# Kernel tuning notes

Hardware: AMD Instinct MI355X
Metric: run time of the kernel (lower is better)

Reference implementation:

```python
import jax, jax.numpy as jnp
import numpy as np


def gcn_conv(h, edge_index, num_nodes):
    # Symmetric-normalized GCN aggregation: out[i] = sum_{(j->i)} h[j] / sqrt(deg(i)*deg(j))
    row, col = edge_index[0], edge_index[1]
    deg = jax.ops.segment_sum(jnp.ones(col.shape, dtype=h.dtype), col, num_segments=num_nodes)
    d_inv_sqrt = jnp.where(deg > 0, jax.lax.rsqrt(jnp.maximum(deg, 1.0)), 0.0)
    w = d_inv_sqrt[row] * d_inv_sqrt[col]           # [E]
    msg = h[row] * w[:, None]                        # [E, D] gather + scale
    return jax.ops.segment_sum(msg, col, num_segments=num_nodes)  # [N, D] scatter-add


def setup_inputs() -> dict:
    key = jax.random.key(0)
    k1, k2, k3, k4 = jax.random.split(key, 4)
    N, E, F_IN, F_HID, F_OUT = 100000, 1600000, 128, 64, 40
    x = jax.random.normal(k1, (N, F_IN), dtype=jnp.float32)
    edge_index = jax.random.randint(k2, (2, E), 0, N, dtype=jnp.int64)
    # xavier_uniform with gain=1.414 (as in reset_parameters); biases zero
    def xavier(k, shape, gain=1.414):
        fan_out, fan_in = shape
        a = gain * np.sqrt(6.0 / (fan_in + fan_out))
        return jax.random.uniform(k, shape, jnp.float32, -a, a)
    W1 = xavier(k3, (F_HID, F_IN))
    b1 = jnp.zeros((F_HID,), dtype=jnp.float32)
    W2 = xavier(k4, (F_OUT, F_HID))
    b2 = jnp.zeros((F_OUT,), dtype=jnp.float32)
    return {"x": x, "edge_index": edge_index, "W1": W1, "b1": b1, "W2": W2, "b2": b2}


def reference(x, edge_index, W1, b1, W2, b2):
    # GNN.forward with num_layers=2, use_mp=True, eval mode (dropout inactive)
    N = x.shape[0]
    h = x @ W1.T                      # [N, nhid]
    h = gcn_conv(h, edge_index, N)
    h = jax.nn.relu(h + b1)
    h = h @ W2.T                      # [N, nclass]
    h = gcn_conv(h, edge_index, N)
    return h + b2
```

## Files before the change

kernel.cpp:

```cpp
#include <hip/hip_runtime.h>
#include <hip/hip_fp16.h>


typedef __attribute__((ext_vector_type(8))) _Float16 half8v;
typedef __attribute__((ext_vector_type(4))) float   float4v;

__global__ void k_binfill(const int* __restrict__ ed,
                          int* __restrict__ gbincnt, unsigned* __restrict__ binbuf,
                          int E, int cap) {
  __shared__ int hist[512];
  __shared__ int cursor[512];
  __shared__ unsigned rec[4096];
  __shared__ unsigned short binv[4096];
  __shared__ int s_is64;
  int t = threadIdx.x;
  hist[t] = 0; hist[t + 256] = 0;
  if (t == 0) s_is64 = 1;
  __syncthreads();
  {
    int any = 0;
    #pragma unroll
    for (int u = 0; u < 8; ++u) {
      int idx = 2 * (t * 8 + u) + 1;
      if (idx < 2 * E && ed[idx] != 0) any = 1;
    }
    if (any) s_is64 = 0;
  }
  __syncthreads();
  const int is64 = s_is64;
  const int base = blockIdx.x * 4096;
  const int nE = min(4096, E - base);
  for (int j = t; j < nE; j += 256) {
    int e = base + j;
    int r = is64 ? ed[2 * e] : ed[e];
    int c = is64 ? ed[2 * (E + e)] : ed[E + e];
    rec[j] = (unsigned)r | ((unsigned)(c & 255) << 17);
    binv[j] = (unsigned short)(c >> 8);
    atomicAdd(&hist[c >> 8], 1);
  }
  __syncthreads();
  for (int b = t; b < 512; b += 256) {
    int h = hist[b];
    cursor[b] = h ? atomicAdd(&gbincnt[b], h) : 0;
  }
  __syncthreads();
  for (int j = t; j < nE; j += 256) {
    int bin = binv[j];
    int pos = atomicAdd(&cursor[bin], 1);
    if (pos < cap)
      binbuf[(size_t)bin * cap + pos] = rec[j];
  }
}

__global__ void k_degscat(const unsigned* __restrict__ binbuf, const int* __restrict__ gbincnt,
                          float* __restrict__ dis, int* __restrict__ rowptr,
                          int* __restrict__ srcs, int NBINS, int N, int cap) {
  __shared__ int sd[512];
  __shared__ int cnt[256];
  __shared__ int sc[256];
  __shared__ int cursor[256];
  __shared__ unsigned rec[8192];
  int t = threadIdx.x, b = blockIdx.x;
  sd[t]       = (t < NBINS)       ? min(gbincnt[t], cap)       : 0;
  sd[t + 256] = (t + 256 < NBINS) ? min(gbincnt[t + 256], cap) : 0;
  cnt[t] = 0;
  __syncthreads();
  for (int off = 1; off < 512; off <<= 1) {
    int v0 = (t >= off) ? sd[t - off] : 0;
    int v1 = sd[t + 256 - off];
    __syncthreads();
    sd[t] += v0; sd[t + 256] += v1;
    __syncthreads();
  }
  const int mybase = (b == 0) ? 0 : sd[b - 1];
  if (b == NBINS - 1 && t == 0) rowptr[N] = sd[NBINS - 1];

  int n = min(gbincnt[b], cap);
  const unsigned* buf = binbuf + (size_t)b * cap;
  for (int j = t; j < n; j += 256) {
    unsigned v = buf[j];
    rec[j] = v;
    atomicAdd(&cnt[v >> 17], 1);
  }
  __syncthreads();
  sc[t] = cnt[t];
  __syncthreads();
  for (int off = 1; off < 256; off <<= 1) {
    int v = (t >= off) ? sc[t - off] : 0;
    __syncthreads();
    sc[t] += v;
    __syncthreads();
  }
  int rp = mybase + ((t == 0) ? 0 : sc[t - 1]);
  cursor[t] = rp;
  int node = b * 256 + t;
  if (node < N) {
    int d = cnt[t];
    dis[node] = (d > 0) ? rsqrtf((float)d) : 0.f;
    rowptr[node] = rp;
  }
  __syncthreads();
  for (int j = t; j < n; j += 256) {
    unsigned v = rec[j];
    int pos = atomicAdd(&cursor[v >> 17], 1);
    srcs[pos] = (int)(v & 0x1FFFF);
  }
}

__launch_bounds__(256)
__global__ void k_gemm1_mfma(const float* __restrict__ X, const float* __restrict__ W,
                             const float* __restrict__ dis, unsigned char* __restrict__ h1q,
                             float* __restrict__ sc1, int N) {
  __shared__ _Float16 xl[128 * 128];
  __shared__ _Float16 wl[64 * 128];
  const int t = threadIdx.x;
  const int row0 = blockIdx.x * 128;

  #pragma unroll
  for (int j = 0; j < 8; ++j) {
    int qq = t + 256 * j;
    int r = qq >> 5, k4 = qq & 31;
    float4 v = *(const float4*)&W[(size_t)r * 128 + k4 * 4];
    _Float16 h4[4] = {(_Float16)v.x, (_Float16)v.y, (_Float16)v.z, (_Float16)v.w};
    int k = (k4 * 4) ^ ((r & 7) * 8);
    *(float2*)&wl[r * 128 + k] = *(float2*)h4;
  }
  #pragma unroll
  for (int j = 0; j < 16; ++j) {
    int qq = t + 256 * j;
    int r = qq >> 5, k4 = qq & 31;
    int row = row0 + r;
    float4 v = make_float4(0.f, 0.f, 0.f, 0.f);
    if (row < N) v = *(const float4*)&X[(size_t)row * 128 + k4 * 4];
    _Float16 h4[4] = {(_Float16)v.x, (_Float16)v.y, (_Float16)v.z, (_Float16)v.w};
    int k = (k4 * 4) ^ ((r & 7) * 8);
    *(float2*)&xl[r * 128 + k] = *(float2*)h4;
  }
  __syncthreads();

  const int w = t >> 6, l = t & 63;
  const int m0 = w * 32;
  const int lr = l & 15, q = l >> 4;

  float4v acc[2][4] = {};
  #pragma unroll
  for (int kc = 0; kc < 4; ++kc) {
    half8v a[2], b[4];
    #pragma unroll
    for (int mt = 0; mt < 2; ++mt) {
      int m = m0 + mt * 16 + lr;
      int k = (kc * 32 + q * 8) ^ ((m & 7) * 8);
      a[mt] = *(half8v*)&xl[m * 128 + k];
    }
    #pragma unroll
    for (int nt = 0; nt < 4; ++nt) {
      int n = nt * 16 + lr;
      int k = (kc * 32 + q * 8) ^ ((n & 7) * 8);
      b[nt] = *(half8v*)&wl[n * 128 + k];
    }
    #pragma unroll
    for (int mt = 0; mt < 2; ++mt)
      #pragma unroll
      for (int nt = 0; nt < 4; ++nt)
        acc[mt][nt] = __builtin_amdgcn_mfma_f32_16x16x32_f16(a[mt], b[nt], acc[mt][nt], 0, 0, 0);
  }

  #pragma unroll
  for (int mt = 0; mt < 2; ++mt) {
    #pragma unroll
    for (int r = 0; r < 4; ++r) {
      int row = row0 + m0 + mt * 16 + q * 4 + r;
      if (row < N) {
        float dr = dis[row];
        float v0 = acc[mt][0][r] * dr;
        float v1 = acc[mt][1][r] * dr;
        float v2 = acc[mt][2][r] * dr;
        float v3 = acc[mt][3][r] * dr;
        float m = fmaxf(fmaxf(fabsf(v0), fabsf(v1)), fmaxf(fabsf(v2), fabsf(v3)));
        #pragma unroll
        for (int off = 1; off < 16; off <<= 1)
          m = fmaxf(m, __shfl_xor(m, off));
        float inv = (m > 0.f) ? (127.f / m) : 0.f;
        unsigned char* dst = h1q + (size_t)row * 64;
        int q0 = (int)rintf(v0 * inv);
        int q1 = (int)rintf(v1 * inv);
        int q2 = (int)rintf(v2 * inv);
        int q3 = (int)rintf(v3 * inv);
        q0 = max(-127, min(127, q0));
        q1 = max(-127, min(127, q1));
        q2 = max(-127, min(127, q2));
        q3 = max(-127, min(127, q3));
        dst[lr]      = (unsigned char)(signed char)q0;
        dst[lr + 16] = (unsigned char)(signed char)q1;
        dst[lr + 32] = (unsigned char)(signed char)q2;
        dst[lr + 48] = (unsigned char)(signed char)q3;
        if (lr == 0) sc1[row] = m * (1.f / 127.f);
      }
    }
  }
}

__launch_bounds__(256)
__global__ void k_gemm2_mfma(const __half* __restrict__ Xh, const float* __restrict__ W,
                             const float* __restrict__ dis, unsigned char* __restrict__ h2,
                             int N) {
  __shared__ _Float16 xl[128 * 64];
  __shared__ _Float16 wl[48 * 64];
  const int t = threadIdx.x;
  const int row0 = blockIdx.x * 128;

  for (int i = t; i < 48 * 8; i += 256) {
    int c = i >> 3, kq = i & 7;
    _Float16 h8[8];
    #pragma unroll
    for (int j = 0; j < 8; ++j)
      h8[j] = (c < 40) ? (_Float16)W[c * 64 + kq * 8 + j] : (_Float16)0.f;
    *(float4*)&wl[c * 64 + ((kq * 8) ^ ((c & 7) * 8))] = *(float4*)h8;
  }
  for (int i = t; i < 1024; i += 256) {
    int r = i >> 3, kq = i & 7;
    int row = row0 + r;
    float4 v = make_float4(0.f, 0.f, 0.f, 0.f);
    if (row < N) v = *(const float4*)&Xh[(size_t)row * 64 + kq * 8];
    *(float4*)&xl[r * 64 + ((kq * 8) ^ ((r & 7) * 8))] = v;
  }
  __syncthreads();

  const int w = t >> 6, l = t & 63;
  const int m0 = w * 32;
  const int lr = l & 15, q = l >> 4;

  float4v acc[2][3] = {};
  #pragma unroll
  for (int kc = 0; kc < 2; ++kc) {
    half8v a[2], b[3];
    #pragma unroll
    for (int mt = 0; mt < 2; ++mt) {
      int m = m0 + mt * 16 + lr;
      int k = (kc * 32 + q * 8) ^ ((m & 7) * 8);
      a[mt] = *(half8v*)&xl[m * 64 + k];
    }
    #pragma unroll
    for (int nt = 0; nt < 3; ++nt) {
      int n = nt * 16 + lr;
      int k = (kc * 32 + q * 8) ^ ((n & 7) * 8);
      b[nt] = *(half8v*)&wl[n * 64 + k];
    }
    #pragma unroll
    for (int mt = 0; mt < 2; ++mt)
      #pragma unroll
      for (int nt = 0; nt < 3; ++nt)
        acc[mt][nt] = __builtin_amdgcn_mfma_f32_16x16x32_f16(a[mt], b[nt], acc[mt][nt], 0, 0, 0);
  }

  #pragma unroll
  for (int mt = 0; mt < 2; ++mt) {
    #pragma unroll
    for (int r = 0; r < 4; ++r) {
      int row = row0 + m0 + mt * 16 + q * 4 + r;
      if (row < N) {
        float dr = dis[row];
        float v0 = acc[mt][0][r] * dr;
        float v1 = acc[mt][1][r] * dr;
        float v2 = acc[mt][2][r] * dr;
        float m = fmaxf(fabsf(v0), fmaxf(fabsf(v1), fabsf(v2)));
        #pragma unroll
        for (int off = 1; off < 16; off <<= 1)
          m = fmaxf(m, __shfl_xor(m, off));
        float s = m * (1.f / 127.f);
        float inv = (m > 0.f) ? (127.f / m) : 0.f;
        unsigned char* dst = h2 + (size_t)row * 64;
        int q0 = (int)rintf(v0 * inv);
        int q1 = (int)rintf(v1 * inv);
        int q2 = (int)rintf(v2 * inv);
        q0 = max(-127, min(127, q0));
        q1 = max(-127, min(127, q1));
        q2 = max(-127, min(127, q2));
        dst[lr]      = (unsigned char)(signed char)q0;
        dst[lr + 16] = (unsigned char)(signed char)q1;
        if (lr + 32 < 40) dst[lr + 32] = (unsigned char)(signed char)q2;
        if (lr == 0) *(float*)&dst[40] = s;
        if (lr >= 1 && lr <= 5) *(int*)&dst[40 + 4 * lr] = 0;
      }
    }
  }
}

__launch_bounds__(256)
__global__ void k_conv64(const unsigned char* __restrict__ H, const float* __restrict__ sc1,
                         const int* __restrict__ rowptr, const int* __restrict__ srcs,
                         const float* __restrict__ dis, const float* __restrict__ b1,
                         __half* __restrict__ out, int N) {
  int node = blockIdx.x * 4 + (threadIdx.x >> 6);
  if (node >= N) return;
  int lane = threadIdx.x & 63;
  int g = lane >> 3, li = lane & 7;
  int s = rowptr[node], e = rowptr[node + 1];
  int last = e - 1;
  float a0 = 0.f, a1 = 0.f, a2 = 0.f, a3 = 0.f,
        a4 = 0.f, a5 = 0.f, a6 = 0.f, a7 = 0.f;
  for (int p = s; p < e; p += 32) {
    int sv = srcs[min(p + (lane & 31), last)];
    #pragma unroll
    for (int u = 0; u < 4; ++u) {
      if (p + 8 * u >= e) break;
      int src = __shfl(sv, 8 * u + g);
      uint2 raw = *(const uint2*)&H[(size_t)src * 64 + 8 * li];
      float sc = sc1[src];
      if (p + 8 * u + g < e) {
        int x0 = (int)raw.x, x1 = (int)raw.y;
        a0 = fmaf((float)((x0 << 24) >> 24), sc, a0);
        a1 = fmaf((float)((x0 << 16) >> 24), sc, a1);
        a2 = fmaf((float)((x0 << 8)  >> 24), sc, a2);
        a3 = fmaf((float)( x0        >> 24), sc, a3);
        a4 = fmaf((float)((x1 << 24) >> 24), sc, a4);
        a5 = fmaf((float)((x1 << 16) >> 24), sc, a5);
        a6 = fmaf((float)((x1 << 8)  >> 24), sc, a6);
        a7 = fmaf((float)( x1        >> 24), sc, a7);
      }
    }
  }
  #pragma unroll
  for (int off = 8; off <= 32; off <<= 1) {
    a0 += __shfl_xor(a0, off); a1 += __shfl_xor(a1, off);
    a2 += __shfl_xor(a2, off); a3 += __shfl_xor(a3, off);
    a4 += __shfl_xor(a4, off); a5 += __shfl_xor(a5, off);
    a6 += __shfl_xor(a6, off); a7 += __shfl_xor(a7, off);
  }
  if (g == 0) {
    float dn = dis[node];
    const float* bb = b1 + 8 * li;
    __half hv[8];
    hv[0] = __float2half_rn(fmaxf(fmaf(a0, dn, bb[0]), 0.f));
    hv[1] = __float2half_rn(fmaxf(fmaf(a1, dn, bb[1]), 0.f));
    hv[2] = __float2half_rn(fmaxf(fmaf(a2, dn, bb[2]), 0.f));
    hv[3] = __float2half_rn(fmaxf(fmaf(a3, dn, bb[3]), 0.f));
    hv[4] = __float2half_rn(fmaxf(fmaf(a4, dn, bb[4]), 0.f));
    hv[5] = __float2half_rn(fmaxf(fmaf(a5, dn, bb[5]), 0.f));
    hv[6] = __float2half_rn(fmaxf(fmaf(a6, dn, bb[6]), 0.f));
    hv[7] = __float2half_rn(fmaxf(fmaf(a7, dn, bb[7]), 0.f));
    *(float4*)&out[(size_t)node * 64 + 8 * li] = *(float4*)hv;
  }
}

__launch_bounds__(256)
__global__ void k_conv40(const unsigned char* __restrict__ H, const int* __restrict__ rowptr,
                         const int* __restrict__ srcs, const float* __restrict__ dis,
                         const float* __restrict__ b2, float* __restrict__ out, int N) {
  int node = blockIdx.x * 4 + (threadIdx.x >> 6);
  if (node >= N) return;
  int lane = threadIdx.x & 63;
  int g = lane >> 3, li = lane & 7;
  bool act = li < 5;
  int s = rowptr[node], e = rowptr[node + 1];
  int last = e - 1;
  float a0 = 0.f, a1 = 0.f, a2 = 0.f, a3 = 0.f,
        a4 = 0.f, a5 = 0.f, a6 = 0.f, a7 = 0.f;
  for (int p = s; p < e; p += 32) {
    int sv = srcs[min(p + (lane & 31), last)];
    #pragma unroll
    for (int u = 0; u < 4; ++u) {
      if (p + 8 * u >= e) break;
      int src = __shfl(sv, 8 * u + g);
      if (act) {
        const unsigned char* rowp = &H[(size_t)src * 64];
        uint2 raw = *(const uint2*)&rowp[8 * li];
        float sc = *(const float*)&rowp[40];
        if (p + 8 * u + g < e) {
          int x0 = (int)raw.x, x1 = (int)raw.y;
          a0 = fmaf((float)((x0 << 24) >> 24), sc, a0);
          a1 = fmaf((float)((x0 << 16) >> 24), sc, a1);
          a2 = fmaf((float)((x0 << 8)  >> 24), sc, a2);
          a3 = fmaf((float)( x0        >> 24), sc, a3);
          a4 = fmaf((float)((x1 << 24) >> 24), sc, a4);
          a5 = fmaf((float)((x1 << 16) >> 24), sc, a5);
          a6 = fmaf((float)((x1 << 8)  >> 24), sc, a6);
          a7 = fmaf((float)( x1        >> 24), sc, a7);
        }
      }
    }
  }
  #pragma unroll
  for (int off = 8; off <= 32; off <<= 1) {
    a0 += __shfl_xor(a0, off); a1 += __shfl_xor(a1, off);
    a2 += __shfl_xor(a2, off); a3 += __shfl_xor(a3, off);
    a4 += __shfl_xor(a4, off); a5 += __shfl_xor(a5, off);
    a6 += __shfl_xor(a6, off); a7 += __shfl_xor(a7, off);
  }
  if (g == 0 && act) {
    float dn = dis[node];
    const float* bb = b2 + 8 * li;
    float4 v0 = make_float4(fmaf(a0, dn, bb[0]), fmaf(a1, dn, bb[1]),
                            fmaf(a2, dn, bb[2]), fmaf(a3, dn, bb[3]));
    float4 v1 = make_float4(fmaf(a4, dn, bb[4]), fmaf(a5, dn, bb[5]),
                            fmaf(a6, dn, bb[6]), fmaf(a7, dn, bb[7]));
    *(float4*)&out[(size_t)node * 40 + 8 * li] = v0;
    *(float4*)&out[(size_t)node * 40 + 8 * li + 4] = v1;
  }
}

extern "C" void kernel_launch(void* const* d_in, const int* in_sizes, int n_in,
                              void* d_out, int out_size, void* d_ws, size_t ws_size,
                              hipStream_t stream) {
  const float* x  = (const float*)d_in[0];
  const int*   ed = (const int*)d_in[1];
  const float* W1 = (const float*)d_in[2];
  const float* b1 = (const float*)d_in[3];
  const float* W2 = (const float*)d_in[4];
  const float* b2 = (const float*)d_in[5];
  float* out = (float*)d_out;

  const int FIN = 128, FH = 64;
  const int N = in_sizes[0] / FIN;
  const int E = in_sizes[1] / 2;
  const int NBINS = (N + 255) >> 8;

  char* ws = (char*)d_ws;
  size_t off = 0;
  auto alloc = [&](size_t bytes) {
    void* p = ws + off;
    off = (off + bytes + 255) & ~(size_t)255;
    return p;
  };
  int*           gbincnt = (int*)alloc(512 * 4);
  float*         dis     = (float*)alloc((size_t)N * 4);
  int*           rowptr  = (int*)alloc(((size_t)N + 1) * 4);
  int*           srcs    = (int*)alloc((size_t)E * 4);
  unsigned char* h1q     = (unsigned char*)alloc((size_t)N * FH * 2);
  __half*        h1b     = (__half*)alloc((size_t)N * FH * 2);
  unsigned char* h2      = (unsigned char*)alloc((size_t)N * 64);
  float* sc1 = (float*)(h1q + (((size_t)N * 64 + 255) & ~(size_t)255));
  int cap = (int)(((size_t)N * FH * 2) / ((size_t)NBINS * 4));
  if (cap > 8192) cap = 8192;
  unsigned* binbuf = (unsigned*)h1q;

  hipMemsetAsync(gbincnt, 0, 512 * 4, stream);

  int fb = (E + 4095) / 4096;
  k_binfill<<<fb, 256, 0, stream>>>(ed, gbincnt, binbuf, E, cap);
  k_degscat<<<NBINS, 256, 0, stream>>>(binbuf, gbincnt, dis, rowptr, srcs, NBINS, N, cap);

  int mb = (N + 127) / 128;
  int cb = (N + 3) / 4;
  k_gemm1_mfma<<<mb, 256, 0, stream>>>(x, W1, dis, h1q, sc1, N);
  k_conv64<<<cb, 256, 0, stream>>>(h1q, sc1, rowptr, srcs, dis, b1, h1b, N);
  k_gemm2_mfma<<<mb, 256, 0, stream>>>(h1b, W2, dis, h2, N);
  k_conv40<<<cb, 256, 0, stream>>>(h2, rowptr, srcs, dis, b2, out, N);
}
```

Baseline: 253.7 us.

## Assign one 8-lane group per node in GCN aggregation kernels

Both aggregation kernels now map each node to 8 lanes instead of a full 64-lane wavefront. Each group walks its edge list 4 at a time with direct index loads, and the cross-group shuffle reduction is gone. With about 16 edges per node, the old scheme left most of the 8 groups idle in the tail of each 32-edge chunk and spent time on shuffles. The cost is divergence between the 8 nodes sharing a wave when their degrees differ, and less memory parallelism per node.

Measured after the change: 232.6 us. 1.09x faster.

```diff
diff --git a/kernel.cpp b/kernel.cpp
--- a/kernel.cpp
+++ b/kernel.cpp
@@ -291,103 +291,161 @@
                          const int* __restrict__ rowptr, const int* __restrict__ srcs,
                          const float* __restrict__ dis, const float* __restrict__ b1,
                          __half* __restrict__ out, int N) {
-  int node = blockIdx.x * 4 + (threadIdx.x >> 6);
+  int t = threadIdx.x;
+  int li = t & 7;
+  int node = blockIdx.x * 32 + (t >> 3);
   if (node >= N) return;
-  int lane = threadIdx.x & 63;
-  int g = lane >> 3, li = lane & 7;
   int s = rowptr[node], e = rowptr[node + 1];
   int last = e - 1;
   float a0 = 0.f, a1 = 0.f, a2 = 0.f, a3 = 0.f,
         a4 = 0.f, a5 = 0.f, a6 = 0.f, a7 = 0.f;
-  for (int p = s; p < e; p += 32) {
-    int sv = srcs[min(p + (lane & 31), last)];
-    #pragma unroll
-    for (int u = 0; u < 4; ++u) {
-      if (p + 8 * u >= e) break;
-      int src = __shfl(sv, 8 * u + g);
-      uint2 raw = *(const uint2*)&H[(size_t)src * 64 + 8 * li];
-      float sc = sc1[src];
-      if (p + 8 * u + g < e) {
-        int x0 = (int)raw.x, x1 = (int)raw.y;
-        a0 = fmaf((float)((x0 << 24) >> 24), sc, a0);
-        a1 = fmaf((float)((x0 << 16) >> 24), sc, a1);
-        a2 = fmaf((float)((x0 << 8)  >> 24), sc, a2);
-        a3 = fmaf((float)( x0        >> 24), sc, a3);
-        a4 = fmaf((float)((x1 << 24) >> 24), sc, a4);
-        a5 = fmaf((float)((x1 << 16) >> 24), sc, a5);
-        a6 = fmaf((float)((x1 << 8)  >> 24), sc, a6);
-        a7 = fmaf((float)( x1        >> 24), sc, a7);
-      }
-    }
-  }
-  #pragma unroll
-  for (int off = 8; off <= 32; off <<= 1) {
-    a0 += __shfl_xor(a0, off); a1 += __shfl_xor(a1, off);
-    a2 += __shfl_xor(a2, off); a3 += __shfl_xor(a3, off);
-    a4 += __shfl_xor(a4, off); a5 += __shfl_xor(a5, off);
-    a6 += __shfl_xor(a6, off); a7 += __shfl_xor(a7, off);
-  }
-  if (g == 0) {
-    float dn = dis[node];
-    const float* bb = b1 + 8 * li;
-    __half hv[8];
-    hv[0] = __float2half_rn(fmaxf(fmaf(a0, dn, bb[0]), 0.f));
-    hv[1] = __float2half_rn(fmaxf(fmaf(a1, dn, bb[1]), 0.f));
-    hv[2] = __float2half_rn(fmaxf(fmaf(a2, dn, bb[2]), 0.f));
-    hv[3] = __float2half_rn(fmaxf(fmaf(a3, dn, bb[3]), 0.f));
-    hv[4] = __float2half_rn(fmaxf(fmaf(a4, dn, bb[4]), 0.f));
-    hv[5] = __float2half_rn(fmaxf(fmaf(a5, dn, bb[5]), 0.f));
-    hv[6] = __float2half_rn(fmaxf(fmaf(a6, dn, bb[6]), 0.f));
-    hv[7] = __float2half_rn(fmaxf(fmaf(a7, dn, bb[7]), 0.f));
-    *(float4*)&out[(size_t)node * 64 + 8 * li] = *(float4*)hv;
-  }
+  for (int p = s; p < e; p += 4) {
+    int s0 = srcs[p];
+    int s1 = srcs[min(p + 1, last)];
+    int s2 = srcs[min(p + 2, last)];
+    int s3 = srcs[min(p + 3, last)];
+    uint2 r0 = *(const uint2*)&H[(size_t)s0 * 64 + 8 * li];
+    uint2 r1 = *(const uint2*)&H[(size_t)s1 * 64 + 8 * li];
+    uint2 r2 = *(const uint2*)&H[(size_t)s2 * 64 + 8 * li];
+    uint2 r3 = *(const uint2*)&H[(size_t)s3 * 64 + 8 * li];
+    float c0 = sc1[s0], c1 = sc1[s1], c2 = sc1[s2], c3 = sc1[s3];
+    {
+      int x0 = (int)r0.x, x1 = (int)r0.y;
+      a0 = fmaf((float)((x0 << 24) >> 24), c0, a0);
+      a1 = fmaf((float)((x0 << 16) >> 24), c0, a1);
+      a2 = fmaf((float)((x0 << 8)  >> 24), c0, a2);
+      a3 = fmaf((float)( x0        >> 24), c0, a3);
+      a4 = fmaf((float)((x1 << 24) >> 24), c0, a4);
+      a5 = fmaf((float)((x1 << 16) >> 24), c0, a5);
+      a6 = fmaf((float)((x1 << 8)  >> 24), c0, a6);
+      a7 = fmaf((float)( x1        >> 24), c0, a7);
+    }
+    if (p + 1 < e) {
+      int x0 = (int)r1.x, x1 = (int)r1.y;
+      a0 = fmaf((float)((x0 << 24) >> 24), c1, a0);
+      a1 = fmaf((float)((x0 << 16) >> 24), c1, a1);
+      a2 = fmaf((float)((x0 << 8)  >> 24), c1, a2);
+      a3 = fmaf((float)( x0        >> 24), c1, a3);
+      a4 = fmaf((float)((x1 << 24) >> 24), c1, a4);
+      a5 = fmaf((float)((x1 << 16) >> 24), c1, a5);
+      a6 = fmaf((float)((x1 << 8)  >> 24), c1, a6);
+      a7 = fmaf((float)( x1        >> 24), c1, a7);
+    }
+    if (p + 2 < e) {
+      int x0 = (int)r2.x, x1 = (int)r2.y;
+      a0 = fmaf((float)((x0 << 24) >> 24), c2, a0);
+      a1 = fmaf((float)((x0 << 16) >> 24), c2, a1);
+      a2 = fmaf((float)((x0 << 8)  >> 24), c2, a2);
+      a3 = fmaf((float)( x0        >> 24), c2, a3);
+      a4 = fmaf((float)((x1 << 24) >> 24), c2, a4);
+      a5 = fmaf((float)((x1 << 16) >> 24), c2, a5);
+      a6 = fmaf((float)((x1 << 8)  >> 24), c2, a6);
+      a7 = fmaf((float)( x1        >> 24), c2, a7);
+    }
+    if (p + 3 < e) {
+      int x0 = (int)r3.x, x1 = (int)r3.y;
+      a0 = fmaf((float)((x0 << 24) >> 24), c3, a0);
+      a1 = fmaf((float)((x0 << 16) >> 24), c3, a1);
+      a2 = fmaf((float)((x0 << 8)  >> 24), c3, a2);
+      a3 = fmaf((float)( x0        >> 24), c3, a3);
+      a4 = fmaf((float)((x1 << 24) >> 24), c3, a4);
+      a5 = fmaf((float)((x1 << 16) >> 24), c3, a5);
+      a6 = fmaf((float)((x1 << 8)  >> 24), c3, a6);
+      a7 = fmaf((float)( x1        >> 24), c3, a7);
+    }
+  }
+  float dn = dis[node];
+  const float* bb = b1 + 8 * li;
+  __half hv[8];
+  hv[0] = __float2half_rn(fmaxf(fmaf(a0, dn, bb[0]), 0.f));
+  hv[1] = __float2half_rn(fmaxf(fmaf(a1, dn, bb[1]), 0.f));
+  hv[2] = __float2half_rn(fmaxf(fmaf(a2, dn, bb[2]), 0.f));
+  hv[3] = __float2half_rn(fmaxf(fmaf(a3, dn, bb[3]), 0.f));
+  hv[4] = __float2half_rn(fmaxf(fmaf(a4, dn, bb[4]), 0.f));
+  hv[5] = __float2half_rn(fmaxf(fmaf(a5, dn, bb[5]), 0.f));
+  hv[6] = __float2half_rn(fmaxf(fmaf(a6, dn, bb[6]), 0.f));
+  hv[7] = __float2half_rn(fmaxf(fmaf(a7, dn, bb[7]), 0.f));
+  *(float4*)&out[(size_t)node * 64 + 8 * li] = *(float4*)hv;
 }
 
 __launch_bounds__(256)
 __global__ void k_conv40(const unsigned char* __restrict__ H, const int* __restrict__ rowptr,
                          const int* __restrict__ srcs, const float* __restrict__ dis,
                          const float* __restrict__ b2, float* __restrict__ out, int N) {
-  int node = blockIdx.x * 4 + (threadIdx.x >> 6);
+  int t = threadIdx.x;
+  int li = t & 7;
+  int node = blockIdx.x * 32 + (t >> 3);
   if (node >= N) return;
-  int lane = threadIdx.x & 63;
-  int g = lane >> 3, li = lane & 7;
   bool act = li < 5;
   int s = rowptr[node], e = rowptr[node + 1];
   int last = e - 1;
   float a0 = 0.f, a1 = 0.f, a2 = 0.f, a3 = 0.f,
         a4 = 0.f, a5 = 0.f, a6 = 0.f, a7 = 0.f;
-  for (int p = s; p < e; p += 32) {
-    int sv = srcs[min(p + (lane & 31), last)];
-    #pragma unroll
-    for (int u = 0; u < 4; ++u) {
-      if (p + 8 * u >= e) break;
-      int src = __shfl(sv, 8 * u + g);
-      if (act) {
-        const unsigned char* rowp = &H[(size_t)src * 64];
-        uint2 raw = *(const uint2*)&rowp[8 * li];
-        float sc = *(const float*)&rowp[40];
-        if (p + 8 * u + g < e) {
-          int x0 = (int)raw.x, x1 = (int)raw.y;
-          a0 = fmaf((float)((x0 << 24) >> 24), sc, a0);
-          a1 = fmaf((float)((x0 << 16) >> 24), sc, a1);
-          a2 = fmaf((float)((x0 << 8)  >> 24), sc, a2);
-          a3 = fmaf((float)( x0        >> 24), sc, a3);
-          a4 = fmaf((float)((x1 << 24) >> 24), sc, a4);
-          a5 = fmaf((float)((x1 << 16) >> 24), sc, a5);
-          a6 = fmaf((float)((x1 << 8)  >> 24), sc, a6);
-          a7 = fmaf((float)( x1        >> 24), sc, a7);
-        }
+  for (int p = s; p < e; p += 4) {
+    int s0 = srcs[p];
+    int s1 = srcs[min(p + 1, last)];
+    int s2 = srcs[min(p + 2, last)];
+    int s3 = srcs[min(p + 3, last)];
+    if (act) {
+      const unsigned char* p0 = &H[(size_t)s0 * 64];
+      const unsigned char* p1 = &H[(size_t)s1 * 64];
+      const unsigned char* p2 = &H[(size_t)s2 * 64];
+      const unsigned char* p3 = &H[(size_t)s3 * 64];
+      uint2 r0 = *(const uint2*)&p0[8 * li];
+      uint2 r1 = *(const uint2*)&p1[8 * li];
+      uint2 r2 = *(const uint2*)&p2[8 * li];
+      uint2 r3 = *(const uint2*)&p3[8 * li];
+      float c0 = *(const float*)&p0[40];
+      float c1 = *(const float*)&p1[40];
+      float c2 = *(const float*)&p2[40];
+      float c3 = *(const float*)&p3[40];
+      {
+        int x0 = (int)r0.x, x1 = (int)r0.y;
+        a0 = fmaf((float)((x0 << 24) >> 24), c0, a0);
+        a1 = fmaf((float)((x0 << 16) >> 24), c0, a1);
+        a2 = fmaf((float)((x0 << 8)  >> 24), c0, a2);
+        a3 = fmaf((float)( x0        >> 24), c0, a3);
+        a4 = fmaf((float)((x1 << 24) >> 24), c0, a4);
+        a5 = fmaf((float)((x1 << 16) >> 24), c0, a5);
+        a6 = fmaf((float)((x1 << 8)  >> 24), c0, a6);
+        a7 = fmaf((float)( x1        >> 24), c0, a7);
       }
-    }
-  }
-  #pragma unroll
-  for (int off = 8; off <= 32; off <<= 1) {
-    a0 += __shfl_xor(a0, off); a1 += __shfl_xor(a1, off);
-    a2 += __shfl_xor(a2, off); a3 += __shfl_xor(a3, off);
-    a4 += __shfl_xor(a4, off); a5 += __shfl_xor(a5, off);
-    a6 += __shfl_xor(a6, off); a7 += __shfl_xor(a7, off);
-  }
-  if (g == 0 && act) {
+      if (p + 1 < e) {
+        int x0 = (int)r1.x, x1 = (int)r1.y;
+        a0 = fmaf((float)((x0 << 24) >> 24), c1, a0);
+        a1 = fmaf((float)((x0 << 16) >> 24), c1, a1);
+        a2 = fmaf((float)((x0 << 8)  >> 24), c1, a2);
+        a3 = fmaf((float)( x0        >> 24), c1, a3);
+        a4 = fmaf((float)((x1 << 24) >> 24), c1, a4);
+        a5 = fmaf((float)((x1 << 16) >> 24), c1, a5);
+        a6 = fmaf((float)((x1 << 8)  >> 24), c1, a6);
+        a7 = fmaf((float)( x1        >> 24), c1, a7);
+      }
+      if (p + 2 < e) {
+        int x0 = (int)r2.x, x1 = (int)r2.y;
+        a0 = fmaf((float)((x0 << 24) >> 24), c2, a0);
+        a1 = fmaf((float)((x0 << 16) >> 24), c2, a1);
+        a2 = fmaf((float)((x0 << 8)  >> 24), c2, a2);
+        a3 = fmaf((float)( x0        >> 24), c2, a3);
+        a4 = fmaf((float)((x1 << 24) >> 24), c2, a4);
+        a5 = fmaf((float)((x1 << 16) >> 24), c2, a5);
+        a6 = fmaf((float)((x1 << 8)  >> 24), c2, a6);
+        a7 = fmaf((float)( x1        >> 24), c2, a7);
+      }
+      if (p + 3 < e) {
+        int x0 = (int)r3.x, x1 = (int)r3.y;
+        a0 = fmaf((float)((x0 << 24) >> 24), c3, a0);
+        a1 = fmaf((float)((x0 << 16) >> 24), c3, a1);
+        a2 = fmaf((float)((x0 << 8)  >> 24), c3, a2);
+        a3 = fmaf((float)( x0        >> 24), c3, a3);
+        a4 = fmaf((float)((x1 << 24) >> 24), c3, a4);
+        a5 = fmaf((float)((x1 << 16) >> 24), c3, a5);
+        a6 = fmaf((float)((x1 << 8)  >> 24), c3, a6);
+        a7 = fmaf((float)( x1        >> 24), c3, a7);
+      }
+    }
+  }
+  if (act) {
     float dn = dis[node];
     const float* bb = b2 + 8 * li;
     float4 v0 = make_float4(fmaf(a0, dn, bb[0]), fmaf(a1, dn, bb[1]),
@@ -441,7 +499,7 @@
   k_degscat<<<NBINS, 256, 0, stream>>>(binbuf, gbincnt, dis, rowptr, srcs, NBINS, N, cap);
 
   int mb = (N + 127) / 128;
-  int cb = (N + 3) / 4;
+  int cb = (N + 31) / 32;
   k_gemm1_mfma<<<mb, 256, 0, stream>>>(x, W1, dis, h1q, sc1, N);
   k_conv64<<<cb, 256, 0, stream>>>(h1q, sc1, rowptr, srcs, dis, b1, h1b, N);
   k_gemm2_mfma<<<mb, 256, 0, stream>>>(h1b, W2, dis, h2, N);
```

## Assign one 8-lane group per node in conv kernels; load GEMM1 A operands directly

Applied to the files above, without the earlier changes.

The two aggregation kernels now map 8 lanes to each destination node, with 32 nodes per block, where before a full 64-lane wavefront served one node. Each lane walks all of the node's edges in batches of 8 with independent loads, and the cross-group shuffle reduction is removed. This aims to stop wasting lanes on low-degree nodes (average degree about 16) and to raise memory-level parallelism. Separately, GEMM1 loads X rows straight from global memory into registers in MFMA operand layout, skipping the shared-memory staging of X. The costs are higher register pressure and divergence across nodes of different degree within a wavefront.

Result: faster. 219.4 us (-13.5%).

```diff
diff --git a/kernel.cpp b/kernel.cpp
--- a/kernel.cpp
+++ b/kernel.cpp
@@ -111,10 +111,24 @@
 __global__ void k_gemm1_mfma(const float* __restrict__ X, const float* __restrict__ W,
                              const float* __restrict__ dis, unsigned char* __restrict__ h1q,
                              float* __restrict__ sc1, int N) {
-  __shared__ _Float16 xl[128 * 128];
   __shared__ _Float16 wl[64 * 128];
   const int t = threadIdx.x;
   const int row0 = blockIdx.x * 128;
+  const int w = t >> 6, l = t & 63;
+  const int m0 = w * 32;
+  const int lr = l & 15, q = l >> 4;
+
+  float4 xr[4][2][2];
+  #pragma unroll
+  for (int kc = 0; kc < 4; ++kc) {
+    #pragma unroll
+    for (int mt = 0; mt < 2; ++mt) {
+      int row = min(row0 + m0 + mt * 16 + lr, N - 1);
+      const float* p = &X[(size_t)row * 128 + kc * 32 + q * 8];
+      xr[kc][mt][0] = *(const float4*)p;
+      xr[kc][mt][1] = *(const float4*)(p + 4);
+    }
+  }
 
   #pragma unroll
   for (int j = 0; j < 8; ++j) {
@@ -125,22 +139,7 @@
     int k = (k4 * 4) ^ ((r & 7) * 8);
     *(float2*)&wl[r * 128 + k] = *(float2*)h4;
   }
-  #pragma unroll
-  for (int j = 0; j < 16; ++j) {
-    int qq = t + 256 * j;
-    int r = qq >> 5, k4 = qq & 31;
-    int row = row0 + r;
-    float4 v = make_float4(0.f, 0.f, 0.f, 0.f);
-    if (row < N) v = *(const float4*)&X[(size_t)row * 128 + k4 * 4];
-    _Float16 h4[4] = {(_Float16)v.x, (_Float16)v.y, (_Float16)v.z, (_Float16)v.w};
-    int k = (k4 * 4) ^ ((r & 7) * 8);
-    *(float2*)&xl[r * 128 + k] = *(float2*)h4;
-  }
-  __syncthreads();
-
-  const int w = t >> 6, l = t & 63;
-  const int m0 = w * 32;
-  const int lr = l & 15, q = l >> 4;
+  __syncthreads();
 
   float4v acc[2][4] = {};
   #pragma unroll
@@ -148,9 +147,10 @@
     half8v a[2], b[4];
     #pragma unroll
     for (int mt = 0; mt < 2; ++mt) {
-      int m = m0 + mt * 16 + lr;
-      int k = (kc * 32 + q * 8) ^ ((m & 7) * 8);
-      a[mt] = *(half8v*)&xl[m * 128 + k];
+      float4 v0 = xr[kc][mt][0], v1 = xr[kc][mt][1];
+      _Float16 h8[8] = {(_Float16)v0.x, (_Float16)v0.y, (_Float16)v0.z, (_Float16)v0.w,
+                        (_Float16)v1.x, (_Float16)v1.y, (_Float16)v1.z, (_Float16)v1.w};
+      a[mt] = *(half8v*)h8;
     }
     #pragma unroll
     for (int nt = 0; nt < 4; ++nt) {
@@ -291,103 +291,95 @@
                          const int* __restrict__ rowptr, const int* __restrict__ srcs,
                          const float* __restrict__ dis, const float* __restrict__ b1,
                          __half* __restrict__ out, int N) {
-  int node = blockIdx.x * 4 + (threadIdx.x >> 6);
+  int t = threadIdx.x;
+  int li = t & 7;
+  int node = blockIdx.x * 32 + (t >> 3);
   if (node >= N) return;
-  int lane = threadIdx.x & 63;
-  int g = lane >> 3, li = lane & 7;
   int s = rowptr[node], e = rowptr[node + 1];
   int last = e - 1;
   float a0 = 0.f, a1 = 0.f, a2 = 0.f, a3 = 0.f,
         a4 = 0.f, a5 = 0.f, a6 = 0.f, a7 = 0.f;
-  for (int p = s; p < e; p += 32) {
-    int sv = srcs[min(p + (lane & 31), last)];
-    #pragma unroll
-    for (int u = 0; u < 4; ++u) {
-      if (p + 8 * u >= e) break;
-      int src = __shfl(sv, 8 * u + g);
-      uint2 raw = *(const uint2*)&H[(size_t)src * 64 + 8 * li];
-      float sc = sc1[src];
-      if (p + 8 * u + g < e) {
-        int x0 = (int)raw.x, x1 = (int)raw.y;
-        a0 = fmaf((float)((x0 << 24) >> 24), sc, a0);
-        a1 = fmaf((float)((x0 << 16) >> 24), sc, a1);
-        a2 = fmaf((float)((x0 << 8)  >> 24), sc, a2);
-        a3 = fmaf((float)( x0        >> 24), sc, a3);
-        a4 = fmaf((float)((x1 << 24) >> 24), sc, a4);
-        a5 = fmaf((float)((x1 << 16) >> 24), sc, a5);
-        a6 = fmaf((float)((x1 << 8)  >> 24), sc, a6);
-        a7 = fmaf((float)( x1        >> 24), sc, a7);
+  for (int p = s; p < e; p += 8) {
+    int sv[8]; uint2 rv[8]; float cv[8];
+    #pragma unroll
+    for (int u = 0; u < 8; ++u) sv[u] = srcs[min(p + u, last)];
+    #pragma unroll
+    for (int u = 0; u < 8; ++u) rv[u] = *(const uint2*)&H[(size_t)sv[u] * 64 + 8 * li];
+    #pragma unroll
+    for (int u = 0; u < 8; ++u) cv[u] = sc1[sv[u]];
+    #pragma unroll
+    for (int u = 0; u < 8; ++u) {
+      if (p + u < e) {
+        int x0 = (int)rv[u].x, x1 = (int)rv[u].y;
+        float c = cv[u];
+        a0 = fmaf((float)((x0 << 24) >> 24), c, a0);
+        a1 = fmaf((float)((x0 << 16) >> 24), c, a1);
+        a2 = fmaf((float)((x0 << 8)  >> 24), c, a2);
+        a3 = fmaf((float)( x0        >> 24), c, a3);
+        a4 = fmaf((float)((x1 << 24) >> 24), c, a4);
+        a5 = fmaf((float)((x1 << 16) >> 24), c, a5);
+        a6 = fmaf((float)((x1 << 8)  >> 24), c, a6);
+        a7 = fmaf((float)( x1        >> 24), c, a7);
       }
     }
   }
-  #pragma unroll
-  for (int off = 8; off <= 32; off <<= 1) {
-    a0 += __shfl_xor(a0, off); a1 += __shfl_xor(a1, off);
-    a2 += __shfl_xor(a2, off); a3 += __shfl_xor(a3, off);
-    a4 += __shfl_xor(a4, off); a5 += __shfl_xor(a5, off);
-    a6 += __shfl_xor(a6, off); a7 += __shfl_xor(a7, off);
-  }
-  if (g == 0) {
-    float dn = dis[node];
-    const float* bb = b1 + 8 * li;
-    __half hv[8];
-    hv[0] = __float2half_rn(fmaxf(fmaf(a0, dn, bb[0]), 0.f));
-    hv[1] = __float2half_rn(fmaxf(fmaf(a1, dn, bb[1]), 0.f));
-    hv[2] = __float2half_rn(fmaxf(fmaf(a2, dn, bb[2]), 0.f));
-    hv[3] = __float2half_rn(fmaxf(fmaf(a3, dn, bb[3]), 0.f));
-    hv[4] = __float2half_rn(fmaxf(fmaf(a4, dn, bb[4]), 0.f));
-    hv[5] = __float2half_rn(fmaxf(fmaf(a5, dn, bb[5]), 0.f));
-    hv[6] = __float2half_rn(fmaxf(fmaf(a6, dn, bb[6]), 0.f));
-    hv[7] = __float2half_rn(fmaxf(fmaf(a7, dn, bb[7]), 0.f));
-    *(float4*)&out[(size_t)node * 64 + 8 * li] = *(float4*)hv;
-  }
+  float dn = dis[node];
+  const float* bb = b1 + 8 * li;
+  __half hv[8];
+  hv[0] = __float2half_rn(fmaxf(fmaf(a0, dn, bb[0]), 0.f));
+  hv[1] = __float2half_rn(fmaxf(fmaf(a1, dn, bb[1]), 0.f));
+  hv[2] = __float2half_rn(fmaxf(fmaf(a2, dn, bb[2]), 0.f));
+  hv[3] = __float2half_rn(fmaxf(fmaf(a3, dn, bb[3]), 0.f));
+  hv[4] = __float2half_rn(fmaxf(fmaf(a4, dn, bb[4]), 0.f));
+  hv[5] = __float2half_rn(fmaxf(fmaf(a5, dn, bb[5]), 0.f));
+  hv[6] = __float2half_rn(fmaxf(fmaf(a6, dn, bb[6]), 0.f));
+  hv[7] = __float2half_rn(fmaxf(fmaf(a7, dn, bb[7]), 0.f));
+  *(float4*)&out[(size_t)node * 64 + 8 * li] = *(float4*)hv;
 }
 
 __launch_bounds__(256)
 __global__ void k_conv40(const unsigned char* __restrict__ H, const int* __restrict__ rowptr,
                          const int* __restrict__ srcs, const float* __restrict__ dis,
                          const float* __restrict__ b2, float* __restrict__ out, int N) {
-  int node = blockIdx.x * 4 + (threadIdx.x >> 6);
+  int t = threadIdx.x;
+  int li = t & 7;
+  int node = blockIdx.x * 32 + (t >> 3);
   if (node >= N) return;
-  int lane = threadIdx.x & 63;
-  int g = lane >> 3, li = lane & 7;
   bool act = li < 5;
   int s = rowptr[node], e = rowptr[node + 1];
   int last = e - 1;
   float a0 = 0.f, a1 = 0.f, a2 = 0.f, a3 = 0.f,
         a4 = 0.f, a5 = 0.f, a6 = 0.f, a7 = 0.f;
-  for (int p = s; p < e; p += 32) {
-    int sv = srcs[min(p + (lane & 31), last)];
-    #pragma unroll
-    for (int u = 0; u < 4; ++u) {
-      if (p + 8 * u >= e) break;
-      int src = __shfl(sv, 8 * u + g);
-      if (act) {
-        const unsigned char* rowp = &H[(size_t)src * 64];
-        uint2 raw = *(const uint2*)&rowp[8 * li];
-        float sc = *(const float*)&rowp[40];
-        if (p + 8 * u + g < e) {
-          int x0 = (int)raw.x, x1 = (int)raw.y;
-          a0 = fmaf((float)((x0 << 24) >> 24), sc, a0);
-          a1 = fmaf((float)((x0 << 16) >> 24), sc, a1);
-          a2 = fmaf((float)((x0 << 8)  >> 24), sc, a2);
-          a3 = fmaf((float)( x0        >> 24), sc, a3);
-          a4 = fmaf((float)((x1 << 24) >> 24), sc, a4);
-          a5 = fmaf((float)((x1 << 16) >> 24), sc, a5);
-          a6 = fmaf((float)((x1 << 8)  >> 24), sc, a6);
-          a7 = fmaf((float)( x1        >> 24), sc, a7);
+  for (int p = s; p < e; p += 8) {
+    int sv[8];
+    #pragma unroll
+    for (int u = 0; u < 8; ++u) sv[u] = srcs[min(p + u, last)];
+    if (act) {
+      uint2 rv[8]; float cv[8];
+      #pragma unroll
+      for (int u = 0; u < 8; ++u)
+        rv[u] = *(const uint2*)&H[(size_t)sv[u] * 64 + 8 * li];
+      #pragma unroll
+      for (int u = 0; u < 8; ++u)
+        cv[u] = *(const float*)&H[(size_t)sv[u] * 64 + 40];
+      #pragma unroll
+      for (int u = 0; u < 8; ++u) {
+        if (p + u < e) {
+          int x0 = (int)rv[u].x, x1 = (int)rv[u].y;
+          float c = cv[u];
+          a0 = fmaf((float)((x0 << 24) >> 24), c, a0);
+          a1 = fmaf((float)((x0 << 16) >> 24), c, a1);
+          a2 = fmaf((float)((x0 << 8)  >> 24), c, a2);
+          a3 = fmaf((float)( x0        >> 24), c, a3);
+          a4 = fmaf((float)((x1 << 24) >> 24), c, a4);
+          a5 = fmaf((float)((x1 << 16) >> 24), c, a5);
+          a6 = fmaf((float)((x1 << 8)  >> 24), c, a6);
+          a7 = fmaf((float)( x1        >> 24), c, a7);
         }
       }
     }
   }
-  #pragma unroll
-  for (int off = 8; off <= 32; off <<= 1) {
-    a0 += __shfl_xor(a0, off); a1 += __shfl_xor(a1, off);
-    a2 += __shfl_xor(a2, off); a3 += __shfl_xor(a3, off);
-    a4 += __shfl_xor(a4, off); a5 += __shfl_xor(a5, off);
-    a6 += __shfl_xor(a6, off); a7 += __shfl_xor(a7, off);
-  }
-  if (g == 0 && act) {
+  if (act) {
     float dn = dis[node];
     const float* bb = b2 + 8 * li;
     float4 v0 = make_float4(fmaf(a0, dn, bb[0]), fmaf(a1, dn, bb[1]),
@@ -441,7 +433,7 @@
   k_degscat<<<NBINS, 256, 0, stream>>>(binbuf, gbincnt, dis, rowptr, srcs, NBINS, N, cap);
 
   int mb = (N + 127) / 128;
-  int cb = (N + 3) / 4;
+  int cb = (N + 31) / 32;
   k_gemm1_mfma<<<mb, 256, 0, stream>>>(x, W1, dis, h1q, sc1, N);
   k_conv64<<<cb, 256, 0, stream>>>(h1q, sc1, rowptr, srcs, dis, b1, h1b, N);
   k_gemm2_mfma<<<mb, 256, 0, stream>>>(h1b, W2, dis, h2, N);
```
